# Kernel tuning notes

Hardware: AMD Instinct MI355X
Metric: run time of the kernel (lower is better)

## Reference

```python
import jax, jax.numpy as jnp
import numpy as np

B, SQ, HID, NH, PAST = 8, 16, 1024, 16, 4096
DH = HID // NH
ROPE_BASE = 10000.0


def _rope(x, pos):
    # rotate-half RoPE applied over the full hidden dim (as in the module, rope
    # is built with hidden_size and applied before the head split)
    half = x.shape[-1] // 2
    inv_freq = 1.0 / (ROPE_BASE ** (jnp.arange(half, dtype=jnp.float32) / half))
    ang = pos[..., None].astype(jnp.float32) * inv_freq  # [B, S, half]
    cos, sin = jnp.cos(ang), jnp.sin(ang)
    x1, x2 = x[..., :half], x[..., half:]
    return jnp.concatenate([x1 * cos - x2 * sin, x2 * cos + x1 * sin], axis=-1).astype(x.dtype)


def setup_inputs() -> dict:
    key = jax.random.key(0)
    ks = jax.random.split(key, 16)
    s = 1.0 / np.sqrt(HID)
    return {
        "hidden_state": jax.random.normal(ks[0], (B, SQ, HID), jnp.float32),
        "attention_mask": jnp.zeros((B, SQ, SQ), jnp.float32),
        "past_key": jax.random.normal(ks[1], (B, NH, PAST, DH), jnp.float32),
        "past_value": jax.random.normal(ks[2], (B, NH, PAST, DH), jnp.float32),
        "position_ids": jax.random.randint(ks[3], (B, SQ), 0, 4200, jnp.int32),
        "Wq": jax.random.normal(ks[4], (HID, HID), jnp.float32) * s,
        "bq": jnp.zeros((HID,), jnp.float32),
        "Wk": jax.random.normal(ks[5], (HID, HID), jnp.float32) * s,
        "bk": jnp.zeros((HID,), jnp.float32),
        "Wv": jax.random.normal(ks[6], (HID, HID), jnp.float32) * s,
        "bv": jnp.zeros((HID,), jnp.float32),
        "Wo": jax.random.normal(ks[7], (HID, HID), jnp.float32) * s,
        "bo": jnp.zeros((HID,), jnp.float32),
    }


def reference(hidden_state, attention_mask, past_key, past_value, position_ids,
              Wq, bq, Wk, bk, Wv, bv, Wo, bo):
    b, sq, hid = hidden_state.shape
    nh = NH
    dh = hid // nh

    q = hidden_state @ Wq + bq
    k = hidden_state @ Wk + bk
    v = hidden_state @ Wv + bv

    q = _rope(q, position_ids)
    k = _rope(k, position_ids)

    # split heads -> [B, H, S, Dh]
    q = q.reshape(b, sq, nh, dh).transpose(0, 2, 1, 3)
    k = k.reshape(b, sq, nh, dh).transpose(0, 2, 1, 3)
    v = v.reshape(b, sq, nh, dh).transpose(0, 2, 1, 3)

    # KV-cache concat along the key/seq dim
    new_key = jnp.concatenate((past_key, k), axis=2)      # [B, H, Skv, Dh]
    new_value = jnp.concatenate((past_value, v), axis=2)
    skv_past = past_key.shape[2]
    mask = jnp.concatenate(
        (jnp.zeros((b, sq, skv_past), attention_mask.dtype), attention_mask), axis=2)

    scale = 1.0 / jnp.sqrt(jnp.asarray(dh, q.dtype))
    scores = jnp.einsum("bhqd,bhkd->bhqk", q, new_key) * scale + mask[:, None]
    probs = jax.nn.softmax(scores, axis=-1)
    ctx = jnp.einsum("bhqk,bhkd->bhqd", probs, new_value)  # [B, H, Sq, Dh]

    out = ctx.transpose(0, 2, 1, 3).reshape(b, sq, hid) @ Wo + bo
    return (out, new_key, new_value)
```

## Files before the change

kernel.cpp:

```cpp
#include <hip/hip_runtime.h>
#include <math.h>

#define BB   8
#define SQ   16
#define HIDD 1024
#define NHD  16
#define PAST 4096
#define DH   64
#define SKV  (PAST + SQ)
#define NTOK (BB * SQ)

__global__ __launch_bounds__(256) void gemm3(
    const float* __restrict__ A,
    const float* __restrict__ W0, const float* __restrict__ W1, const float* __restrict__ W2,
    const float* __restrict__ b0, const float* __restrict__ b1, const float* __restrict__ b2,
    float* __restrict__ O0, float* __restrict__ O1, float* __restrict__ O2)
{
    const int nt   = blockIdx.x;
    const int mt   = blockIdx.y;
    const int wsel = nt >> 4;
    const int col0 = (nt & 15) * 64;
    const int m0   = mt * 32;
    const float* W    = (wsel == 0) ? W0 : (wsel == 1) ? W1 : W2;
    const float* bias = (wsel == 0) ? b0 : (wsel == 1) ? b1 : b2;
    float*       Out  = (wsel == 0) ? O0 : (wsel == 1) ? O1 : O2;

    __shared__ float As[32][33];
    __shared__ float Bs[32][64];

    const int t    = threadIdx.x;
    const int tm   = t >> 4;
    const int tn   = t & 15;
    const int arow = t >> 3;
    const int acol = (t & 7) << 2;
    const int brow = t >> 4;
    const int bcol = (t & 15) << 2;

    float acc0[4] = {0.f,0.f,0.f,0.f};
    float acc1[4] = {0.f,0.f,0.f,0.f};

    float4 ra  = *(const float4*)(A + (size_t)(m0 + arow) * HIDD + acol);
    float4 rb0 = *(const float4*)(W + (size_t)brow        * HIDD + col0 + bcol);
    float4 rb1 = *(const float4*)(W + (size_t)(brow + 16) * HIDD + col0 + bcol);

    for (int k0 = 0; k0 < HIDD; k0 += 32) {
        __syncthreads();
        As[arow][acol+0] = ra.x; As[arow][acol+1] = ra.y;
        As[arow][acol+2] = ra.z; As[arow][acol+3] = ra.w;
        *(float4*)(&Bs[brow][bcol])      = rb0;
        *(float4*)(&Bs[brow + 16][bcol]) = rb1;
        if (k0 + 32 < HIDD) {
            ra  = *(const float4*)(A + (size_t)(m0 + arow) * HIDD + k0 + 32 + acol);
            rb0 = *(const float4*)(W + (size_t)(k0 + 32 + brow) * HIDD + col0 + bcol);
            rb1 = *(const float4*)(W + (size_t)(k0 + 48 + brow) * HIDD + col0 + bcol);
        }
        __syncthreads();
        #pragma unroll
        for (int kk = 0; kk < 32; ++kk) {
            const float  a0 = As[2*tm][kk];
            const float  a1 = As[2*tm + 1][kk];
            const float4 b4 = *(const float4*)(&Bs[kk][tn << 2]);
            acc0[0] += a0*b4.x; acc0[1] += a0*b4.y; acc0[2] += a0*b4.z; acc0[3] += a0*b4.w;
            acc1[0] += a1*b4.x; acc1[1] += a1*b4.y; acc1[2] += a1*b4.z; acc1[3] += a1*b4.w;
        }
    }
    const float4 bb = *(const float4*)(bias + col0 + (tn << 2));
    float* o0 = Out + (size_t)(m0 + 2*tm) * HIDD + col0 + (tn << 2);
    float* o1 = o0 + HIDD;
    o0[0] = acc0[0] + bb.x; o0[1] = acc0[1] + bb.y; o0[2] = acc0[2] + bb.z; o0[3] = acc0[3] + bb.w;
    o1[0] = acc1[0] + bb.x; o1[1] = acc1[1] + bb.y; o1[2] = acc1[2] + bb.z; o1[3] = acc1[3] + bb.w;
}

__global__ __launch_bounds__(256) void rope_scatter(
    const float* __restrict__ qr, const float* __restrict__ kr, const float* __restrict__ vr,
    const int* __restrict__ pos_ids,
    float* __restrict__ Qh, float* __restrict__ nk, float* __restrict__ nv)
{
    const int tok = blockIdx.x;
    const int b   = tok >> 4;
    const int s   = tok & 15;
    const float pos = (float)pos_ids[tok];
    const size_t rq = (size_t)tok * HIDD;
    for (int i = threadIdx.x; i < 512; i += 256) {
        const float inv = __expf((float)i * (-9.210340371976184f / 512.0f));
        const float ang = pos * inv;
        float c, sn;
        __sincosf(ang, &sn, &c);
        const int h1 = i >> 6, d = i & 63;
        const int h2 = h1 + 8;
        float x1, x2;
        x1 = qr[rq + i]; x2 = qr[rq + i + 512];
        Qh[((size_t)(b*NHD + h1)*SQ + s)*DH + d] = x1*c - x2*sn;
        Qh[((size_t)(b*NHD + h2)*SQ + s)*DH + d] = x2*c + x1*sn;
        x1 = kr[rq + i]; x2 = kr[rq + i + 512];
        nk[((size_t)(b*NHD + h1)*SKV + PAST + s)*DH + d] = x1*c - x2*sn;
        nk[((size_t)(b*NHD + h2)*SKV + PAST + s)*DH + d] = x2*c + x1*sn;
        x1 = vr[rq + i]; x2 = vr[rq + i + 512];
        nv[((size_t)(b*NHD + h1)*SKV + PAST + s)*DH + d] = x1;
        nv[((size_t)(b*NHD + h2)*SKV + PAST + s)*DH + d] = x2;
    }
}

__global__ __launch_bounds__(256) void attn_partial(
    const float* __restrict__ pk, const float* __restrict__ pv,
    const float* __restrict__ Qh, const float* __restrict__ amask,
    float* __restrict__ nk, float* __restrict__ nv,
    float* __restrict__ pc, float* __restrict__ pm, float* __restrict__ pl)
{
    const int chunk = blockIdx.x;
    const int bh    = blockIdx.y;
    const int b     = bh >> 4;
    const int t     = threadIdx.x;
    const int w     = t >> 6;
    const int lane  = t & 63;
    const int qq    = lane >> 4;
    const int d4    = lane & 15;

    __shared__ float  Qs[SQ * DH];
    __shared__ float4 Ks[64 * 16];
    __shared__ float  Vs[64 * DH];
    __shared__ float  Ps2[4][4][64];

    const int j0 = t >> 4;
    const int i0 = t & 15;
    const size_t pbase = (size_t)bh * PAST * DH;
    const size_t nbase = (size_t)bh * SKV  * DH;

    float4 ka[4], va[4];
    {
        const int k0 = chunk * 512;
        #pragma unroll
        for (int p = 0; p < 4; ++p) {
            const size_t po = pbase + (size_t)(k0 + j0 + 16*p) * DH + 4*i0;
            ka[p] = *(const float4*)(pk + po);
            va[p] = *(const float4*)(pv + po);
        }
    }

    {
        const int q = t >> 4, i = t & 15;
        float4 q4 = *(const float4*)(Qh + ((size_t)bh * SQ + q) * DH + 4*i);
        q4.x *= 0.125f; q4.y *= 0.125f; q4.z *= 0.125f; q4.w *= 0.125f;
        *(float4*)(&Qs[q * DH + 4*i]) = q4;
    }

    float m_r[4], l_r[4];
    #pragma unroll
    for (int q = 0; q < 4; ++q) { m_r[q] = -3.0e38f; l_r[q] = 0.0f; }
    float4 ctx = make_float4(0.f, 0.f, 0.f, 0.f);

    const int ntiles = (chunk == 7) ? 9 : 8;
    for (int tile = 0; tile < ntiles; ++tile) {
        __syncthreads();
        if (tile < 8) {
            const int k0 = chunk * 512 + tile * 64;
            #pragma unroll
            for (int p = 0; p < 4; ++p) {
                const int j = j0 + 16*p;
                const size_t no = nbase + (size_t)(k0 + j) * DH + 4*i0;
                Ks[j * 16 + (i0 ^ (j & 7))] = ka[p];
                *(float4*)(&Vs[j * DH + 4*i0]) = va[p];
                *(float4*)(nk + no) = ka[p];
                *(float4*)(nv + no) = va[p];
            }
            if (tile < 7) {
                const int k1 = chunk * 512 + (tile + 1) * 64;
                #pragma unroll
                for (int p = 0; p < 4; ++p) {
                    const size_t po = pbase + (size_t)(k1 + j0 + 16*p) * DH + 4*i0;
                    ka[p] = *(const float4*)(pk + po);
                    va[p] = *(const float4*)(pv + po);
                }
            }
        } else {
            const size_t no = nbase + (size_t)(PAST + j0) * DH + 4*i0;
            Ks[j0 * 16 + (i0 ^ (j0 & 7))] = *(const float4*)(nk + no);
            *(float4*)(&Vs[j0 * DH + 4*i0]) = *(const float4*)(nv + no);
        }
        __syncthreads();

        const int jcount = (tile < 8) ? 64 : 16;

        float s[4];
        {
            float4 acc[4];
            #pragma unroll
            for (int q = 0; q < 4; ++q) acc[q] = make_float4(0.f,0.f,0.f,0.f);
            if (lane < jcount) {
                #pragma unroll
                for (int i = 0; i < 16; ++i) {
                    const float4 k4 = Ks[lane * 16 + (i ^ (lane & 7))];
                    #pragma unroll
                    for (int q = 0; q < 4; ++q) {
                        const float4 q4 = *(const float4*)(&Qs[(4*w + q) * DH + 4*i]);
                        acc[q].x += k4.x * q4.x; acc[q].y += k4.y * q4.y;
                        acc[q].z += k4.z * q4.z; acc[q].w += k4.w * q4.w;
                    }
                }
            }
            #pragma unroll
            for (int q = 0; q < 4; ++q)
                s[q] = (lane < jcount) ? (acc[q].x + acc[q].y + acc[q].z + acc[q].w)
                                       : -3.0e38f;
        }
        if (tile == 8 && lane < 16) {
            #pragma unroll
            for (int q = 0; q < 4; ++q)
                s[q] += amask[((size_t)b * SQ + 4*w + q) * SQ + lane];
        }

        float alpha[4], pjv[4];
        #pragma unroll
        for (int q = 0; q < 4; ++q) {
            float mx = s[q];
            #pragma unroll
            for (int off = 1; off < 64; off <<= 1)
                mx = fmaxf(mx, __shfl_xor(mx, off, 64));
            const float mnew = fmaxf(m_r[q], mx);
            alpha[q] = __expf(m_r[q] - mnew);
            const float p = __expf(s[q] - mnew);
            pjv[q] = p;
            float ps = p;
            #pragma unroll
            for (int off = 1; off < 64; off <<= 1)
                ps += __shfl_xor(ps, off, 64);
            l_r[q] = l_r[q] * alpha[q] + ps;
            m_r[q] = mnew;
        }
        #pragma unroll
        for (int q = 0; q < 4; ++q)
            Ps2[w][q][lane] = pjv[q];

        const float asel = (qq == 0) ? alpha[0] : (qq == 1) ? alpha[1]
                         : (qq == 2) ? alpha[2] : alpha[3];
        ctx.x *= asel; ctx.y *= asel; ctx.z *= asel; ctx.w *= asel;

        const float* Pq = &Ps2[w][0][0] + qq * 64;
        const int j4 = jcount >> 2;
        for (int jj = 0; jj < j4; ++jj) {
            const float4 p4 = *(const float4*)(Pq + 4*jj);
            const float4 v0 = *(const float4*)(&Vs[(4*jj + 0) * DH + 4*d4]);
            const float4 v1 = *(const float4*)(&Vs[(4*jj + 1) * DH + 4*d4]);
            const float4 v2 = *(const float4*)(&Vs[(4*jj + 2) * DH + 4*d4]);
            const float4 v3 = *(const float4*)(&Vs[(4*jj + 3) * DH + 4*d4]);
            ctx.x += p4.x*v0.x; ctx.y += p4.x*v0.y; ctx.z += p4.x*v0.z; ctx.w += p4.x*v0.w;
            ctx.x += p4.y*v1.x; ctx.y += p4.y*v1.y; ctx.z += p4.y*v1.z; ctx.w += p4.y*v1.w;
            ctx.x += p4.z*v2.x; ctx.y += p4.z*v2.y; ctx.z += p4.z*v2.z; ctx.w += p4.z*v2.w;
            ctx.x += p4.w*v3.x; ctx.y += p4.w*v3.y; ctx.z += p4.w*v3.z; ctx.w += p4.w*v3.w;
        }
    }

    const int blk = bh * 8 + chunk;
    const int qg  = 4*w + qq;
    *(float4*)(pc + (size_t)blk * 1024 + qg * DH + 4*d4) = ctx;
    if (d4 == 0) {
        const float msel = (qq == 0) ? m_r[0] : (qq == 1) ? m_r[1] : (qq == 2) ? m_r[2] : m_r[3];
        const float lsel = (qq == 0) ? l_r[0] : (qq == 1) ? l_r[1] : (qq == 2) ? l_r[2] : l_r[3];
        pm[blk * 16 + qg] = msel;
        pl[blk * 16 + qg] = lsel;
    }
}

__global__ __launch_bounds__(256) void attn_reduce(
    const float* __restrict__ pc, const float* __restrict__ pm,
    const float* __restrict__ pl, float* __restrict__ ctxw)
{
    const int bh = blockIdx.x;
    const int b  = bh >> 4, h = bh & 15;
    const int t  = threadIdx.x;
    __shared__ float wgt[8][SQ];
    __shared__ float li[SQ];
    if (t < SQ) {
        float m = -3.0e38f;
        #pragma unroll
        for (int c = 0; c < 8; ++c) m = fmaxf(m, pm[(bh*8 + c) * 16 + t]);
        float L = 0.f;
        #pragma unroll
        for (int c = 0; c < 8; ++c) {
            const float e = __expf(pm[(bh*8 + c) * 16 + t] - m);
            L += pl[(bh*8 + c) * 16 + t] * e;
            wgt[c][t] = e;
        }
        li[t] = 1.0f / L;
    }
    __syncthreads();
    #pragma unroll
    for (int r = 0; r < 4; ++r) {
        const int idx = t + 256 * r;
        const int q = idx >> 6, d = idx & 63;
        float acc = 0.f;
        #pragma unroll
        for (int c = 0; c < 8; ++c)
            acc += pc[(size_t)(bh*8 + c) * 1024 + idx] * wgt[c][q];
        ctxw[((size_t)(b*SQ + q) * NHD + h) * DH + d] = acc * li[q];
    }
}

extern "C" void kernel_launch(void* const* d_in, const int* in_sizes, int n_in,
                              void* d_out, int out_size, void* d_ws, size_t ws_size,
                              hipStream_t stream)
{
    const float* hidden = (const float*)d_in[0];
    const float* amask  = (const float*)d_in[1];
    const float* past_k = (const float*)d_in[2];
    const float* past_v = (const float*)d_in[3];
    const int*   pos    = (const int*)  d_in[4];
    const float* Wq = (const float*)d_in[5];  const float* bq = (const float*)d_in[6];
    const float* Wk = (const float*)d_in[7];  const float* bk = (const float*)d_in[8];
    const float* Wv = (const float*)d_in[9];  const float* bv = (const float*)d_in[10];
    const float* Wo = (const float*)d_in[11]; const float* bo = (const float*)d_in[12];

    float* out = (float*)d_out;
    float* nk  = out + (size_t)NTOK * HIDD;
    float* nv  = nk + (size_t)BB * NHD * SKV * DH;

    float* ws     = (float*)d_ws;
    float* q_raw  = ws;
    float* k_raw  = q_raw + 131072;
    float* v_raw  = k_raw + 131072;
    float* Qh     = v_raw + 131072;
    float* pc     = Qh    + 131072;
    float* pm     = pc    + 1024 * 1024;
    float* pl     = pm    + 1024 * 16;
    float* ctxw   = pl    + 1024 * 16;

    gemm3<<<dim3(48, 4), 256, 0, stream>>>(hidden, Wq, Wk, Wv, bq, bk, bv,
                                           q_raw, k_raw, v_raw);
    rope_scatter<<<NTOK, 256, 0, stream>>>(q_raw, k_raw, v_raw, pos, Qh, nk, nv);
    attn_partial<<<dim3(8, 128), 256, 0, stream>>>(past_k, past_v, Qh, amask,
                                                   nk, nv, pc, pm, pl);
    attn_reduce<<<128, 256, 0, stream>>>(pc, pm, pl, ctxw);
    gemm3<<<dim3(16, 4), 256, 0, stream>>>(ctxw, Wo, Wo, Wo, bo, bo, bo,
                                           out, out, out);
}
```

Baseline: 600.7 us.

## Double-buffer shared tiles in projection GEMM and attention loops, one barrier per step

```diff
diff --git a/kernel.cpp b/kernel.cpp
--- a/kernel.cpp
+++ b/kernel.cpp
@@ -10,6 +10,12 @@
 #define SKV  (PAST + SQ)
 #define NTOK (BB * SQ)
 
+#define WAVE_BARRIER() do {                                        \
+    asm volatile("s_waitcnt lgkmcnt(0)" ::: "memory");             \
+    __builtin_amdgcn_s_barrier();                                  \
+    __builtin_amdgcn_sched_barrier(0);                             \
+} while (0)
+
 __global__ __launch_bounds__(256) void gemm3(
     const float* __restrict__ A,
     const float* __restrict__ W0, const float* __restrict__ W1, const float* __restrict__ W2,
@@ -25,8 +31,8 @@
     const float* bias = (wsel == 0) ? b0 : (wsel == 1) ? b1 : b2;
     float*       Out  = (wsel == 0) ? O0 : (wsel == 1) ? O1 : O2;
 
-    __shared__ float As[32][33];
-    __shared__ float Bs[32][64];
+    __shared__ float As[2][32][33];
+    __shared__ float Bs[2][32][64];
 
     const int t    = threadIdx.x;
     const int tm   = t >> 4;
@@ -42,27 +48,38 @@
     float4 ra  = *(const float4*)(A + (size_t)(m0 + arow) * HIDD + acol);
     float4 rb0 = *(const float4*)(W + (size_t)brow        * HIDD + col0 + bcol);
     float4 rb1 = *(const float4*)(W + (size_t)(brow + 16) * HIDD + col0 + bcol);
-
-    for (int k0 = 0; k0 < HIDD; k0 += 32) {
-        __syncthreads();
-        As[arow][acol+0] = ra.x; As[arow][acol+1] = ra.y;
-        As[arow][acol+2] = ra.z; As[arow][acol+3] = ra.w;
-        *(float4*)(&Bs[brow][bcol])      = rb0;
-        *(float4*)(&Bs[brow + 16][bcol]) = rb1;
-        if (k0 + 32 < HIDD) {
-            ra  = *(const float4*)(A + (size_t)(m0 + arow) * HIDD + k0 + 32 + acol);
-            rb0 = *(const float4*)(W + (size_t)(k0 + 32 + brow) * HIDD + col0 + bcol);
-            rb1 = *(const float4*)(W + (size_t)(k0 + 48 + brow) * HIDD + col0 + bcol);
-        }
-        __syncthreads();
+    As[0][arow][acol+0] = ra.x; As[0][arow][acol+1] = ra.y;
+    As[0][arow][acol+2] = ra.z; As[0][arow][acol+3] = ra.w;
+    *(float4*)(&Bs[0][brow][bcol])      = rb0;
+    *(float4*)(&Bs[0][brow + 16][bcol]) = rb1;
+    ra  = *(const float4*)(A + (size_t)(m0 + arow) * HIDD + 32 + acol);
+    rb0 = *(const float4*)(W + (size_t)(32 + brow) * HIDD + col0 + bcol);
+    rb1 = *(const float4*)(W + (size_t)(48 + brow) * HIDD + col0 + bcol);
+    WAVE_BARRIER();
+
+    for (int s = 0; s < 32; ++s) {
+        const int cur = s & 1, nxt = cur ^ 1;
+        if (s + 1 < 32) {
+            As[nxt][arow][acol+0] = ra.x; As[nxt][arow][acol+1] = ra.y;
+            As[nxt][arow][acol+2] = ra.z; As[nxt][arow][acol+3] = ra.w;
+            *(float4*)(&Bs[nxt][brow][bcol])      = rb0;
+            *(float4*)(&Bs[nxt][brow + 16][bcol]) = rb1;
+            if (s + 2 < 32) {
+                const int k2 = (s + 2) * 32;
+                ra  = *(const float4*)(A + (size_t)(m0 + arow) * HIDD + k2 + acol);
+                rb0 = *(const float4*)(W + (size_t)(k2 + brow)      * HIDD + col0 + bcol);
+                rb1 = *(const float4*)(W + (size_t)(k2 + 16 + brow) * HIDD + col0 + bcol);
+            }
+        }
         #pragma unroll
         for (int kk = 0; kk < 32; ++kk) {
-            const float  a0 = As[2*tm][kk];
-            const float  a1 = As[2*tm + 1][kk];
-            const float4 b4 = *(const float4*)(&Bs[kk][tn << 2]);
+            const float  a0 = As[cur][2*tm][kk];
+            const float  a1 = As[cur][2*tm + 1][kk];
+            const float4 b4 = *(const float4*)(&Bs[cur][kk][tn << 2]);
             acc0[0] += a0*b4.x; acc0[1] += a0*b4.y; acc0[2] += a0*b4.z; acc0[3] += a0*b4.w;
             acc1[0] += a1*b4.x; acc1[1] += a1*b4.y; acc1[2] += a1*b4.z; acc1[3] += a1*b4.w;
         }
+        WAVE_BARRIER();
     }
     const float4 bb = *(const float4*)(bias + col0 + (tn << 2));
     float* o0 = Out + (size_t)(m0 + 2*tm) * HIDD + col0 + (tn << 2);
@@ -117,8 +134,8 @@
     const int d4    = lane & 15;
 
     __shared__ float  Qs[SQ * DH];
-    __shared__ float4 Ks[64 * 16];
-    __shared__ float  Vs[64 * DH];
+    __shared__ float4 Ks[2][64 * 16];
+    __shared__ float  Vs[2][64 * DH];
     __shared__ float  Ps2[4][4][64];
 
     const int j0 = t >> 4;
@@ -136,13 +153,37 @@
             va[p] = *(const float4*)(pv + po);
         }
     }
-
+    float4 kt = make_float4(0.f,0.f,0.f,0.f), vt = make_float4(0.f,0.f,0.f,0.f);
+    if (chunk == 7) {
+        const size_t no = nbase + (size_t)(PAST + j0) * DH + 4*i0;
+        kt = *(const float4*)(nk + no);
+        vt = *(const float4*)(nv + no);
+    }
     {
-        const int q = t >> 4, i = t & 15;
-        float4 q4 = *(const float4*)(Qh + ((size_t)bh * SQ + q) * DH + 4*i);
+        float4 q4 = *(const float4*)(Qh + ((size_t)bh * SQ + j0) * DH + 4*i0);
         q4.x *= 0.125f; q4.y *= 0.125f; q4.z *= 0.125f; q4.w *= 0.125f;
-        *(float4*)(&Qs[q * DH + 4*i]) = q4;
-    }
+        *(float4*)(&Qs[j0 * DH + 4*i0]) = q4;
+    }
+    {
+        const int k0 = chunk * 512;
+        #pragma unroll
+        for (int p = 0; p < 4; ++p) {
+            const int j = j0 + 16*p;
+            const size_t no = nbase + (size_t)(k0 + j) * DH + 4*i0;
+            Ks[0][j * 16 + (i0 ^ (j & 7))] = ka[p];
+            *(float4*)(&Vs[0][j * DH + 4*i0]) = va[p];
+            *(float4*)(nk + no) = ka[p];
+            *(float4*)(nv + no) = va[p];
+        }
+        const int k1 = k0 + 64;
+        #pragma unroll
+        for (int p = 0; p < 4; ++p) {
+            const size_t po = pbase + (size_t)(k1 + j0 + 16*p) * DH + 4*i0;
+            ka[p] = *(const float4*)(pk + po);
+            va[p] = *(const float4*)(pv + po);
+        }
+    }
+    WAVE_BARRIER();
 
     float m_r[4], l_r[4];
     #pragma unroll
@@ -151,33 +192,34 @@
 
     const int ntiles = (chunk == 7) ? 9 : 8;
     for (int tile = 0; tile < ntiles; ++tile) {
-        __syncthreads();
-        if (tile < 8) {
-            const int k0 = chunk * 512 + tile * 64;
-            #pragma unroll
-            for (int p = 0; p < 4; ++p) {
-                const int j = j0 + 16*p;
-                const size_t no = nbase + (size_t)(k0 + j) * DH + 4*i0;
-                Ks[j * 16 + (i0 ^ (j & 7))] = ka[p];
-                *(float4*)(&Vs[j * DH + 4*i0]) = va[p];
-                *(float4*)(nk + no) = ka[p];
-                *(float4*)(nv + no) = va[p];
-            }
-            if (tile < 7) {
-                const int k1 = chunk * 512 + (tile + 1) * 64;
+        const int cur = tile & 1, nxt = cur ^ 1;
+
+        if (tile + 1 < ntiles) {
+            if (tile + 1 < 8) {
+                const int k0 = chunk * 512 + (tile + 1) * 64;
                 #pragma unroll
                 for (int p = 0; p < 4; ++p) {
-                    const size_t po = pbase + (size_t)(k1 + j0 + 16*p) * DH + 4*i0;
-                    ka[p] = *(const float4*)(pk + po);
-                    va[p] = *(const float4*)(pv + po);
+                    const int j = j0 + 16*p;
+                    const size_t no = nbase + (size_t)(k0 + j) * DH + 4*i0;
+                    Ks[nxt][j * 16 + (i0 ^ (j & 7))] = ka[p];
+                    *(float4*)(&Vs[nxt][j * DH + 4*i0]) = va[p];
+                    *(float4*)(nk + no) = ka[p];
+                    *(float4*)(nv + no) = va[p];
                 }
+                if (tile + 2 < 8) {
+                    const int k1 = chunk * 512 + (tile + 2) * 64;
+                    #pragma unroll
+                    for (int p = 0; p < 4; ++p) {
+                        const size_t po = pbase + (size_t)(k1 + j0 + 16*p) * DH + 4*i0;
+                        ka[p] = *(const float4*)(pk + po);
+                        va[p] = *(const float4*)(pv + po);
+                    }
+                }
+            } else {
+                Ks[nxt][j0 * 16 + (i0 ^ (j0 & 7))] = kt;
+                *(float4*)(&Vs[nxt][j0 * DH + 4*i0]) = vt;
             }
-        } else {
-            const size_t no = nbase + (size_t)(PAST + j0) * DH + 4*i0;
-            Ks[j0 * 16 + (i0 ^ (j0 & 7))] = *(const float4*)(nk + no);
-            *(float4*)(&Vs[j0 * DH + 4*i0]) = *(const float4*)(nv + no);
-        }
-        __syncthreads();
+        }
 
         const int jcount = (tile < 8) ? 64 : 16;
 
@@ -189,7 +231,7 @@
             if (lane < jcount) {
                 #pragma unroll
                 for (int i = 0; i < 16; ++i) {
-                    const float4 k4 = Ks[lane * 16 + (i ^ (lane & 7))];
+                    const float4 k4 = Ks[cur][lane * 16 + (i ^ (lane & 7))];
                     #pragma unroll
                     for (int q = 0; q < 4; ++q) {
                         const float4 q4 = *(const float4*)(&Qs[(4*w + q) * DH + 4*i]);
@@ -239,15 +281,17 @@
         const int j4 = jcount >> 2;
         for (int jj = 0; jj < j4; ++jj) {
             const float4 p4 = *(const float4*)(Pq + 4*jj);
-            const float4 v0 = *(const float4*)(&Vs[(4*jj + 0) * DH + 4*d4]);
-            const float4 v1 = *(const float4*)(&Vs[(4*jj + 1) * DH + 4*d4]);
-            const float4 v2 = *(const float4*)(&Vs[(4*jj + 2) * DH + 4*d4]);
-            const float4 v3 = *(const float4*)(&Vs[(4*jj + 3) * DH + 4*d4]);
+            const float4 v0 = *(const float4*)(&Vs[cur][(4*jj + 0) * DH + 4*d4]);
+            const float4 v1 = *(const float4*)(&Vs[cur][(4*jj + 1) * DH + 4*d4]);
+            const float4 v2 = *(const float4*)(&Vs[cur][(4*jj + 2) * DH + 4*d4]);
+            const float4 v3 = *(const float4*)(&Vs[cur][(4*jj + 3) * DH + 4*d4]);
             ctx.x += p4.x*v0.x; ctx.y += p4.x*v0.y; ctx.z += p4.x*v0.z; ctx.w += p4.x*v0.w;
             ctx.x += p4.y*v1.x; ctx.y += p4.y*v1.y; ctx.z += p4.y*v1.z; ctx.w += p4.y*v1.w;
             ctx.x += p4.z*v2.x; ctx.y += p4.z*v2.y; ctx.z += p4.z*v2.z; ctx.w += p4.z*v2.w;
             ctx.x += p4.w*v3.x; ctx.y += p4.w*v3.y; ctx.z += p4.w*v3.z; ctx.w += p4.w*v3.w;
         }
+
+        WAVE_BARRIER();
     }
 
     const int blk = bh * 8 + chunk;
```

Result: slower. 631.5 us (+5.1%).
